# Kernel tuning notes

Hardware: AMD Instinct MI355X
Metric: run time of the kernel (lower is better)

## Reference

```python
import jax, jax.numpy as jnp
import numpy as np

B, S, D, F, E = 8, 4096, 512, 2048, 8
INIT_LAMBDA = 0.2
LN_EPS = 1e-5
LN_MERGE = 0.03  # scale used when merging layer_norm expert task-vectors


def setup_inputs() -> dict:
    key = jax.random.key(0)
    ks = jax.random.split(key, 12)
    n = lambda k, shp, s=1.0: jax.random.normal(k, shp, dtype=jnp.float32) * s
    return {
        "hidden_states": n(ks[0], (B, S, D)),
        # DictMoEGate (2 hidden layers): fc1 ~ N(0, 0.01), fc2 bias = init_lambda
        "gfc1_w": n(ks[1], (D, D), 0.01),
        "gfc1_b": jnp.zeros((D,), jnp.float32),
        "gfc2_w": n(ks[2], (E, D), 0.01),
        "gfc2_b": jnp.full((E,), INIT_LAMBDA, dtype=jnp.float32),
        # base PositionWiseFeedForward params (torch Linear layout: [out, in])
        "W1": n(ks[3], (F, D), 0.02),
        "b1": jnp.zeros((F,), jnp.float32),
        "W2": n(ks[4], (D, F), 0.02),
        "b2": jnp.zeros((D,), jnp.float32),
        "ln_g": jnp.ones((D,), jnp.float32),
        "ln_b": jnp.zeros((D,), jnp.float32),
        # expert task vectors (expert_sd - base_sd), one per base param
        "tv_W1": n(ks[5], (E, F, D), 0.02),
        "tv_b1": n(ks[6], (E, F), 0.02),
        "tv_W2": n(ks[7], (E, D, F), 0.02),
        "tv_b2": n(ks[8], (E, D), 0.02),
        "tv_ln_g": n(ks[9], (E, D), 0.02),
        "tv_ln_b": n(ks[10], (E, D), 0.02),
    }


def reference(hidden_states, gfc1_w, gfc1_b, gfc2_w, gfc2_b,
              W1, b1, W2, b2, ln_g, ln_b,
              tv_W1, tv_b1, tv_W2, tv_b2, tv_ln_g, tv_ln_b):
    x = hidden_states  # [B, S, D] (batch_first)
    # --- gate: per-token 2-layer MLP, then mean over sequence -> [B, E] ---
    gh = jax.nn.relu(jnp.einsum('bsd,hd->bsh', x, gfc1_w) + gfc1_b)
    g = (jnp.einsum('bsh,eh->bse', gh, gfc2_w) + gfc2_b).mean(axis=1)  # [B, E]
    # --- per-sample merged weights: base + sum_e g[b,e] * task_vector[e] ---
    W1m = W1 + jnp.einsum('be,efd->bfd', g, tv_W1)   # [B, F, D]
    b1m = b1 + g @ tv_b1                              # [B, F]
    W2m = W2 + jnp.einsum('be,edf->bdf', g, tv_W2)   # [B, D, F]
    b2m = b2 + g @ tv_b2                              # [B, D]
    # layer_norm params: sd = param + sum_e (tv_e - param) * 0.03 (gate-independent)
    lng = ln_g + LN_MERGE * (tv_ln_g - ln_g).sum(axis=0)  # [D]
    lnb = ln_b + LN_MERGE * (tv_ln_b - ln_b).sum(axis=0)  # [D]
    # --- PositionWiseFeedForward with per-sample weights (dropout = eval/identity) ---
    h = jax.nn.relu(jnp.einsum('bsd,bfd->bsf', x, W1m) + b1m[:, None, :])  # [B, S, F]
    out = jnp.einsum('bsf,bdf->bsd', h, W2m) + b2m[:, None, :]             # [B, S, D]
    res = x + out
    mu = res.mean(axis=-1, keepdims=True)
    var = res.var(axis=-1, keepdims=True)
    return (res - mu) * jax.lax.rsqrt(var + LN_EPS) * lng + lnb
```

## Files before the change

### kernel.cpp

```cpp
#include <hip/hip_runtime.h>

typedef __bf16 bf16;
typedef __attribute__((ext_vector_type(8))) __bf16 bf16x8;
typedef __attribute__((ext_vector_type(4))) float f32x4;

#define LDS16(gp, lp)                                                          \
  __builtin_amdgcn_global_load_lds(                                            \
      (const __attribute__((address_space(1))) void*)(gp),                     \
      (__attribute__((address_space(3))) void*)(lp), 16, 0, 0)

__global__ __launch_bounds__(256) void cast_bf16_kernel(const float* __restrict__ src,
                                                        bf16* __restrict__ dst, int n) {
  int i = (blockIdx.x * 256 + threadIdx.x) * 8;
  if (i < n) {
    float4 a = *(const float4*)(src + i);
    float4 b = *(const float4*)(src + i + 4);
    bf16x8 v;
    v[0] = (bf16)a.x; v[1] = (bf16)a.y; v[2] = (bf16)a.z; v[3] = (bf16)a.w;
    v[4] = (bf16)b.x; v[5] = (bf16)b.y; v[6] = (bf16)b.z; v[7] = (bf16)b.w;
    *(bf16x8*)(dst + i) = v;
  }
}

__global__ __launch_bounds__(256) void zero_kernel(float* p, int n) {
  int i = blockIdx.x * 256 + threadIdx.x;
  if (i < n) p[i] = 0.f;
}

template <int MODE, int KTILES>
__global__ __launch_bounds__(256) void gemm_bt(const bf16* __restrict__ A,
                                               const bf16* __restrict__ B0, long bstride,
                                               const float* __restrict__ bias, long biasStride,
                                               const float* __restrict__ resid,
                                               float* __restrict__ fout,
                                               bf16* __restrict__ hout) {
  constexpr int K = KTILES * 64;
  __shared__ bf16 As[128 * 64];
  __shared__ bf16 Bs[128 * 64];
  const int tid = threadIdx.x;
  const int lane = tid & 63, wv = tid >> 6;
  const int wm = wv >> 1, wn = wv & 1;
  const int lr = lane & 15, q = lane >> 4;
  const long blockM = (long)blockIdx.x * 128;
  const int blockN = blockIdx.y * 128;
  const int b = (int)(blockM >> 12);
  const bf16* Bp = B0 + (long)b * bstride;

  f32x4 acc[4][4] = {};

  const bf16* Ab = A + blockM * K;
  const bf16* Bb = Bp + (long)blockN * K;
  const int srow = lane >> 3;
  const int scol = (lane & 7) * 8;

  for (int it = 0; it < KTILES; ++it) {
    const int k0 = it * 64;
#pragma unroll
    for (int c = 0; c < 4; ++c) {
      int n = wv * 4 + c;
      int row = n * 8 + srow;
      LDS16(Ab + (long)row * K + k0 + scol, &As[n * 512]);
      LDS16(Bb + (long)row * K + k0 + scol, &Bs[n * 512]);
    }
    __syncthreads();
#pragma unroll
    for (int ks = 0; ks < 2; ++ks) {
      const int ko = ks * 32 + q * 8;
      bf16x8 af[4], bfr[4];
#pragma unroll
      for (int i = 0; i < 4; ++i)
        af[i] = *(const bf16x8*)&As[(wm * 64 + i * 16 + lr) * 64 + ko];
#pragma unroll
      for (int j = 0; j < 4; ++j)
        bfr[j] = *(const bf16x8*)&Bs[(wn * 64 + j * 16 + lr) * 64 + ko];
#pragma unroll
      for (int i = 0; i < 4; ++i)
#pragma unroll
        for (int j = 0; j < 4; ++j)
          acc[i][j] = __builtin_amdgcn_mfma_f32_16x16x32_bf16(af[i], bfr[j], acc[i][j], 0, 0, 0);
    }
    __syncthreads();
  }

  if (MODE == 0) {
#pragma unroll
    for (int j = 0; j < 4; ++j) {
      const int gc = blockN + wn * 64 + j * 16 + lr;
      const float bv = bias[gc];
      float s = 0.f;
#pragma unroll
      for (int i = 0; i < 4; ++i)
#pragma unroll
        for (int r = 0; r < 4; ++r) {
          float v = acc[i][j][r] + bv;
          s += v > 0.f ? v : 0.f;
        }
      s += __shfl_xor(s, 16);
      s += __shfl_xor(s, 32);
      if (q == 0) atomicAdd(&fout[b * 512 + gc], s);
    }
  } else if (MODE == 1) {
#pragma unroll
    for (int j = 0; j < 4; ++j) {
      const int gc = blockN + wn * 64 + j * 16 + lr;
      const float bv = bias[(long)b * biasStride + gc];
#pragma unroll
      for (int i = 0; i < 4; ++i)
#pragma unroll
        for (int r = 0; r < 4; ++r) {
          const long gr = blockM + wm * 64 + i * 16 + q * 4 + r;
          float v = acc[i][j][r] + bv;
          hout[gr * 2048 + gc] = (bf16)(v > 0.f ? v : 0.f);
        }
    }
  } else {
#pragma unroll
    for (int j = 0; j < 4; ++j) {
      const int gc = blockN + wn * 64 + j * 16 + lr;
      const float bv = bias[(long)b * biasStride + gc];
#pragma unroll
      for (int i = 0; i < 4; ++i)
#pragma unroll
        for (int r = 0; r < 4; ++r) {
          const long gr = blockM + wm * 64 + i * 16 + q * 4 + r;
          fout[gr * 512 + gc] = acc[i][j][r] + bv + resid[gr * 512 + gc];
        }
    }
  }
}

__global__ __launch_bounds__(512) void small_kernel(
    const float* __restrict__ ghsum, const float* __restrict__ g2w,
    const float* __restrict__ g2b, const float* __restrict__ lngI,
    const float* __restrict__ lnbI, const float* __restrict__ tvlg,
    const float* __restrict__ tvlb, const float* __restrict__ b1,
    const float* __restrict__ tvb1, const float* __restrict__ b2,
    const float* __restrict__ tvb2, float* __restrict__ g, float* __restrict__ lng,
    float* __restrict__ lnb, float* __restrict__ b1m, float* __restrict__ b2m) {
  __shared__ float gs[64];
  const int t = threadIdx.x;
  if (t < 64) {
    const int b = t >> 3, e = t & 7;
    float s = 0.f;
    for (int h = 0; h < 512; ++h) s += ghsum[b * 512 + h] * g2w[e * 512 + h];
    float gv = s * (1.f / 4096.f) + g2b[e];
    gs[t] = gv;
    g[t] = gv;
  }
  __syncthreads();
  if (t < 512) {
    float lg = lngI[t], lb = lnbI[t], sg = 0.f, sb = 0.f;
    for (int e = 0; e < 8; ++e) { sg += tvlg[e * 512 + t]; sb += tvlb[e * 512 + t]; }
    lng[t] = lg + 0.03f * (sg - 8.f * lg);
    lnb[t] = lb + 0.03f * (sb - 8.f * lb);
  }
  for (int i = t; i < 8 * 2048; i += 512) {
    const int b = i >> 11, f = i & 2047;
    float s = b1[f];
    for (int e = 0; e < 8; ++e) s += gs[b * 8 + e] * tvb1[e * 2048 + f];
    b1m[i] = s;
  }
  for (int i = t; i < 8 * 512; i += 512) {
    const int b = i >> 9, d = i & 511;
    float s = b2[d];
    for (int e = 0; e < 8; ++e) s += gs[b * 8 + e] * tvb2[e * 512 + d];
    b2m[i] = s;
  }
}

__global__ __launch_bounds__(256) void merge_kernel(
    const float* __restrict__ W1, const float* __restrict__ tvW1,
    const float* __restrict__ W2, const float* __restrict__ tvW2,
    const float* __restrict__ g, bf16* __restrict__ W1m, bf16* __restrict__ W2m) {
  int idx = blockIdx.x * 256 + threadIdx.x;
  if (idx < 1048576) {
    const float w = W1[idx];
    float tv[8];
#pragma unroll
    for (int e = 0; e < 8; ++e) tv[e] = tvW1[(long)e * 1048576 + idx];
#pragma unroll
    for (int b = 0; b < 8; ++b) {
      float s = w;
#pragma unroll
      for (int e = 0; e < 8; ++e) s += g[b * 8 + e] * tv[e];
      W1m[(long)b * 1048576 + idx] = (bf16)s;
    }
  } else {
    idx -= 1048576;
    const float w = W2[idx];
    float tv[8];
#pragma unroll
    for (int e = 0; e < 8; ++e) tv[e] = tvW2[(long)e * 1048576 + idx];
#pragma unroll
    for (int b = 0; b < 8; ++b) {
      float s = w;
#pragma unroll
      for (int e = 0; e < 8; ++e) s += g[b * 8 + e] * tv[e];
      W2m[(long)b * 1048576 + idx] = (bf16)s;
    }
  }
}

__global__ __launch_bounds__(256) void ln_kernel(float* __restrict__ out,
                                                 const float* __restrict__ lng,
                                                 const float* __restrict__ lnb) {
  const int wv = threadIdx.x >> 6, lane = threadIdx.x & 63;
  const long row = (long)blockIdx.x * 4 + wv;
  float* p = out + row * 512 + lane * 8;
  float4 a = *(float4*)p;
  float4 b = *(float4*)(p + 4);
  float v[8] = {a.x, a.y, a.z, a.w, b.x, b.y, b.z, b.w};
  float s1 = 0.f, s2 = 0.f;
#pragma unroll
  for (int k = 0; k < 8; ++k) { s1 += v[k]; s2 += v[k] * v[k]; }
#pragma unroll
  for (int off = 32; off > 0; off >>= 1) {
    s1 += __shfl_xor(s1, off);
    s2 += __shfl_xor(s2, off);
  }
  const float mean = s1 * (1.f / 512.f);
  const float var = s2 * (1.f / 512.f) - mean * mean;
  const float rstd = rsqrtf(var + 1e-5f);
  const int c = lane * 8;
  float o[8];
#pragma unroll
  for (int k = 0; k < 8; ++k) o[k] = (v[k] - mean) * rstd * lng[c + k] + lnb[c + k];
  *(float4*)p = make_float4(o[0], o[1], o[2], o[3]);
  *(float4*)(p + 4) = make_float4(o[4], o[5], o[6], o[7]);
}

extern "C" void kernel_launch(void* const* d_in, const int* in_sizes, int n_in,
                              void* d_out, int out_size, void* d_ws, size_t ws_size,
                              hipStream_t stream) {
  const float* x    = (const float*)d_in[0];
  const float* g1w  = (const float*)d_in[1];
  const float* g1b  = (const float*)d_in[2];
  const float* g2w  = (const float*)d_in[3];
  const float* g2b  = (const float*)d_in[4];
  const float* W1   = (const float*)d_in[5];
  const float* b1   = (const float*)d_in[6];
  const float* W2   = (const float*)d_in[7];
  const float* b2   = (const float*)d_in[8];
  const float* lngI = (const float*)d_in[9];
  const float* lnbI = (const float*)d_in[10];
  const float* tvW1 = (const float*)d_in[11];
  const float* tvb1 = (const float*)d_in[12];
  const float* tvW2 = (const float*)d_in[13];
  const float* tvb2 = (const float*)d_in[14];
  const float* tvlg = (const float*)d_in[15];
  const float* tvlb = (const float*)d_in[16];
  float* out = (float*)d_out;

  char* w = (char*)d_ws;
  bf16*  x_bf   = (bf16*)(w);
  bf16*  g1w_bf = (bf16*)(w + 33554432);
  bf16*  W1m    = (bf16*)(w + 34078720);
  bf16*  W2m    = (bf16*)(w + 50855936);
  bf16*  h      = (bf16*)(w + 67633152);
  float* ghsum  = (float*)(w + 201850880);
  float* g      = (float*)(w + 201867264);
  float* b1m    = (float*)(w + 201867520);
  float* b2m    = (float*)(w + 201933056);
  float* lng    = (float*)(w + 201949440);
  float* lnb    = (float*)(w + 201951488);

  cast_bf16_kernel<<<8192, 256, 0, stream>>>(x, x_bf, 16777216);
  cast_bf16_kernel<<<128, 256, 0, stream>>>(g1w, g1w_bf, 262144);
  zero_kernel<<<16, 256, 0, stream>>>(ghsum, 4096);
  gemm_bt<0, 8><<<dim3(256, 4), 256, 0, stream>>>(x_bf, g1w_bf, 0, g1b, 0,
                                                  nullptr, ghsum, nullptr);
  small_kernel<<<1, 512, 0, stream>>>(ghsum, g2w, g2b, lngI, lnbI, tvlg, tvlb,
                                      b1, tvb1, b2, tvb2, g, lng, lnb, b1m, b2m);
  merge_kernel<<<8192, 256, 0, stream>>>(W1, tvW1, W2, tvW2, g, W1m, W2m);
  gemm_bt<1, 8><<<dim3(256, 16), 256, 0, stream>>>(x_bf, W1m, 1048576, b1m, 2048,
                                                   nullptr, nullptr, h);
  gemm_bt<2, 32><<<dim3(256, 4), 256, 0, stream>>>(h, W2m, 1048576, b2m, 512,
                                                   x, out, nullptr);
  ln_kernel<<<8192, 256, 0, stream>>>(out, lng, lnb);
}
```

Before: 543.9 us.

## Swizzle LDS tiles, stage MODE1 output through LDS, and reorder grid by batch

```diff
diff --git a/kernel.cpp b/kernel.cpp
--- a/kernel.cpp
+++ b/kernel.cpp
@@ -35,15 +35,16 @@
                                                float* __restrict__ fout,
                                                bf16* __restrict__ hout) {
   constexpr int K = KTILES * 64;
-  __shared__ bf16 As[128 * 64];
-  __shared__ bf16 Bs[128 * 64];
+  __shared__ bf16 smem[2 * 128 * 64];
+  bf16* As = smem;
+  bf16* Bs = smem + 8192;
   const int tid = threadIdx.x;
   const int lane = tid & 63, wv = tid >> 6;
   const int wm = wv >> 1, wn = wv & 1;
   const int lr = lane & 15, q = lane >> 4;
-  const long blockM = (long)blockIdx.x * 128;
+  const int b = blockIdx.z;
+  const long blockM = (long)b * 4096 + (long)blockIdx.x * 128;
   const int blockN = blockIdx.y * 128;
-  const int b = (int)(blockM >> 12);
   const bf16* Bp = B0 + (long)b * bstride;
 
   f32x4 acc[4][4] = {};
@@ -51,7 +52,7 @@
   const bf16* Ab = A + blockM * K;
   const bf16* Bb = Bp + (long)blockN * K;
   const int srow = lane >> 3;
-  const int scol = (lane & 7) * 8;
+  const int scol = ((lane & 7) ^ srow) * 8;
 
   for (int it = 0; it < KTILES; ++it) {
     const int k0 = it * 64;
@@ -65,14 +66,15 @@
     __syncthreads();
 #pragma unroll
     for (int ks = 0; ks < 2; ++ks) {
-      const int ko = ks * 32 + q * 8;
+      const int c0 = ks * 4 + q;
+      const int sw = lane & 7;
       bf16x8 af[4], bfr[4];
 #pragma unroll
       for (int i = 0; i < 4; ++i)
-        af[i] = *(const bf16x8*)&As[(wm * 64 + i * 16 + lr) * 64 + ko];
+        af[i] = *(const bf16x8*)&As[(wm * 64 + i * 16 + lr) * 64 + ((c0 ^ sw) * 8)];
 #pragma unroll
       for (int j = 0; j < 4; ++j)
-        bfr[j] = *(const bf16x8*)&Bs[(wn * 64 + j * 16 + lr) * 64 + ko];
+        bfr[j] = *(const bf16x8*)&Bs[(wn * 64 + j * 16 + lr) * 64 + ((c0 ^ sw) * 8)];
 #pragma unroll
       for (int i = 0; i < 4; ++i)
 #pragma unroll
@@ -102,16 +104,24 @@
   } else if (MODE == 1) {
 #pragma unroll
     for (int j = 0; j < 4; ++j) {
-      const int gc = blockN + wn * 64 + j * 16 + lr;
-      const float bv = bias[(long)b * biasStride + gc];
+      const int gc = wn * 64 + j * 16 + lr;
+      const float bv = bias[(long)b * biasStride + blockN + gc];
 #pragma unroll
       for (int i = 0; i < 4; ++i)
 #pragma unroll
         for (int r = 0; r < 4; ++r) {
-          const long gr = blockM + wm * 64 + i * 16 + q * 4 + r;
+          const int lrow = wm * 64 + i * 16 + q * 4 + r;
           float v = acc[i][j][r] + bv;
-          hout[gr * 2048 + gc] = (bf16)(v > 0.f ? v : 0.f);
+          smem[lrow * 128 + gc] = (bf16)(v > 0.f ? v : 0.f);
         }
+    }
+    __syncthreads();
+#pragma unroll
+    for (int p = 0; p < 8; ++p) {
+      const int row = p * 16 + (tid >> 4);
+      const int col = (tid & 15) * 8;
+      *(bf16x8*)&hout[(blockM + row) * 2048 + blockN + col] =
+          *(const bf16x8*)&smem[row * 128 + col];
     }
   } else {
 #pragma unroll
@@ -267,14 +277,14 @@
   cast_bf16_kernel<<<8192, 256, 0, stream>>>(x, x_bf, 16777216);
   cast_bf16_kernel<<<128, 256, 0, stream>>>(g1w, g1w_bf, 262144);
   zero_kernel<<<16, 256, 0, stream>>>(ghsum, 4096);
-  gemm_bt<0, 8><<<dim3(256, 4), 256, 0, stream>>>(x_bf, g1w_bf, 0, g1b, 0,
-                                                  nullptr, ghsum, nullptr);
+  gemm_bt<0, 8><<<dim3(32, 4, 8), 256, 0, stream>>>(x_bf, g1w_bf, 0, g1b, 0,
+                                                    nullptr, ghsum, nullptr);
   small_kernel<<<1, 512, 0, stream>>>(ghsum, g2w, g2b, lngI, lnbI, tvlg, tvlb,
                                       b1, tvb1, b2, tvb2, g, lng, lnb, b1m, b2m);
   merge_kernel<<<8192, 256, 0, stream>>>(W1, tvW1, W2, tvW2, g, W1m, W2m);
-  gemm_bt<1, 8><<<dim3(256, 16), 256, 0, stream>>>(x_bf, W1m, 1048576, b1m, 2048,
-                                                   nullptr, nullptr, h);
-  gemm_bt<2, 32><<<dim3(256, 4), 256, 0, stream>>>(h, W2m, 1048576, b2m, 512,
-                                                   x, out, nullptr);
+  gemm_bt<1, 8><<<dim3(32, 16, 8), 256, 0, stream>>>(x_bf, W1m, 1048576, b1m, 2048,
+                                                     nullptr, nullptr, h);
+  gemm_bt<2, 32><<<dim3(32, 4, 8), 256, 0, stream>>>(h, W2m, 1048576, b2m, 512,
+                                                     x, out, nullptr);
   ln_kernel<<<8192, 256, 0, stream>>>(out, lng, lnb);
 }
```

Measured after the change: 483.6 us. -11.1%, faster.
